# Kernel optimization log

Hardware: AMD Instinct MI355X
Metric: run time of the kernel (lower is better)

## Reference

```python
import jax, jax.numpy as jnp
import numpy as np

N_HEADS = 4

def setup_inputs() -> dict:
    key = jax.random.key(0)
    ks = jax.random.split(key, 9)
    B, C, H, W = 4, 256, 64, 64
    nh, hs = N_HEADS, C // N_HEADS
    s = 0.02
    return {
        "x": jax.random.normal(ks[0], (B, C, H, W), jnp.float32),
        "wq": jax.random.normal(ks[1], (C, C), jnp.float32) * s,
        "bq": jax.random.normal(ks[2], (C,), jnp.float32) * s,
        "wk": jax.random.normal(ks[3], (C, C), jnp.float32) * s,
        "bk": jax.random.normal(ks[4], (C,), jnp.float32) * s,
        "wv": jax.random.normal(ks[5], (C, C), jnp.float32) * s,
        "bv": jax.random.normal(ks[6], (C,), jnp.float32) * s,
        "rel_h": jax.random.normal(ks[7], (1, nh, hs, 1, H), jnp.float32),
        "rel_w": jax.random.normal(ks[8], (1, nh, hs, W, 1), jnp.float32),
    }

def reference(x, wq, bq, wk, bk, wv, bv, rel_h, rel_w):
    B, C, H, W = x.shape
    nh = N_HEADS
    hs = C // nh
    S = H * W

    def proj(w, b):
        # 1x1 conv == per-pixel linear over channels -> [B, C, H, W]
        y = jnp.einsum('oc,bchw->bohw', w, x) + b[None, :, None, None]
        # faithful to torch .view: flatten [C,H,W] row-major into [S, nh, hs]
        y = y.reshape(B, S, nh, hs)
        return y.transpose(0, 2, 1, 3)  # [B, nh, S, hs]

    q = proj(wq, bq)
    k = proj(wk, bk)
    v = proj(wv, bv)

    # content scores (NOTE: no 1/sqrt(d) scaling in BoT override)
    attn_content = jnp.einsum('bnqd,bnkd->bnqk', q, k)  # [B, nh, S, S]
    # learned relative position term: broadcast-add then flatten (w,h) order
    pos = (rel_h + rel_w).reshape(1, nh, hs, S)  # [1, nh, hs, S]
    attn_position = jnp.einsum('bnqd,ands->bnqs', q, pos)  # [B, nh, S, S]

    probs = jax.nn.softmax(attn_content + attn_position, axis=-1)
    ctx = jnp.einsum('bnqk,bnkd->bnqd', probs, v)  # [B, nh, S, hs]
    # faithful to torch: transpose(1,2) then view(B, C, width, height)
    out = ctx.transpose(0, 2, 1, 3).reshape(B, C, W, H)
    return out
```

## Files before the change

### kernel.cpp

```cpp
#include <hip/hip_runtime.h>
#include <hip/hip_bf16.h>
#include <stdint.h>
#include <math.h>

typedef __bf16 bf16_t;
typedef __bf16 bf16x8 __attribute__((ext_vector_type(8)));
typedef float  f32x4  __attribute__((ext_vector_type(4)));
typedef float  f32x16 __attribute__((ext_vector_type(16)));
typedef unsigned int u32;

#define S_SZ 4096
#define HS   64
#define OUT_B_STRIDE (256 * 64 * 64)
#define LOG2E 1.4426950408889634f

#define GLOAD_LDS(gsrc, ldst)                                                              \
    __builtin_amdgcn_global_load_lds((__attribute__((address_space(1))) void*)(void*)(gsrc), \
                                     (__attribute__((address_space(3))) void*)(void*)(ldst),  \
                                     16, 0, 0)

static __device__ __forceinline__ u32 pack2(__bf16 a, __bf16 b) {
    return (u32)__builtin_bit_cast(uint16_t, a) | ((u32)__builtin_bit_cast(uint16_t, b) << 16);
}

__global__ __launch_bounds__(256)
void prep_kernel(const float* __restrict__ wq, const float* __restrict__ wk,
                 const float* __restrict__ wv, const float* __restrict__ rel_h,
                 const float* __restrict__ rel_w,
                 bf16_t* __restrict__ Wh, bf16_t* __restrict__ Wl,
                 bf16_t* __restrict__ Rt)
{
    const int blk = blockIdx.x;
    if (blk < 768) {
        const int o = blk;
        const int c = threadIdx.x;
        const float* src = o < 256 ? wq : (o < 512 ? wk : wv);
        float v = src[(size_t)(o & 255) * 256 + c];
        if (o < 256) v *= LOG2E;
        __bf16 h = (__bf16)v;
        Wh[(size_t)o * 256 + c] = h;
        Wl[(size_t)o * 256 + c] = (__bf16)(v - (float)h);
    } else {
        const int e = (blk - 768) * 256 + threadIdx.x;
        const int n  = e >> 18;
        const int rr = e & 262143;
        const int t  = rr >> 6;
        const int d  = rr & 63;
        const int h2 = t >> 8, o = t & 255;
        float v = rel_h[(n * 64 + d) * 64 + (o & 3) * 16 + h2]
                + rel_w[(n * 64 + d) * 64 + (o >> 2)];
        Rt[e] = (bf16_t)v;
    }
}

__global__ __launch_bounds__(512, 2)
void proj_kernel(const float* __restrict__ x,
                 const bf16_t* __restrict__ Wh, const bf16_t* __restrict__ Wl,
                 const float* __restrict__ bq, const float* __restrict__ bk,
                 const float* __restrict__ bv, const bf16_t* __restrict__ Rt,
                 bf16_t* __restrict__ q_ws, bf16_t* __restrict__ k2_ws,
                 bf16_t* __restrict__ vt2_ws)
{
    const int bx = blockIdx.x;
    const int b  = bx >> 6;
    const int h  = bx & 63;
    const int p0 = h * 64;
    const int n  = h & 3;
    const int h2 = h >> 2;
    const int bn = b * 4 + n;
    const int tid = threadIdx.x;

    __shared__ __align__(16) char SM[65536];

    {
        const int cpair = tid & 127, pg = tid >> 7;
        const int c0 = cpair * 2;
        const float* x0 = x + ((size_t)b * 256 + c0) * 4096 + p0 + pg * 16;
        const int sub = (c0 >> 6) * 128;
        const int u   = (c0 >> 3) & 7;
        const int e2  = (c0 & 7) * 2;
        #pragma unroll
        for (int i4 = 0; i4 < 4; ++i4) {
            f32x4 ra = *(const f32x4*)(x0 + i4 * 4);
            f32x4 rb = *(const f32x4*)(x0 + 4096 + i4 * 4);
            #pragma unroll
            for (int i = 0; i < 4; ++i) {
                const int p = pg * 16 + i4 * 4 + i;
                __bf16 ha = (__bf16)ra[i], hb = (__bf16)rb[i];
                float  la = ra[i] - (float)ha, lb = rb[i] - (float)hb;
                const int off = p * 512 + sub + ((u ^ (p & 7)) * 16) + e2;
                *(u32*)(SM + off)         = pack2(ha, hb);
                *(u32*)(SM + 32768 + off) = pack2((__bf16)la, (__bf16)lb);
            }
        }
    }
    __syncthreads();

    const int wid = tid >> 6, lane = tid & 63, l31 = lane & 31, hi = lane >> 5;

    int obs[3], pjs[3];
    const bf16_t* whp[3];
    const bf16_t* wlp[3];
    #pragma unroll
    for (int j = 0; j < 3; ++j) {
        const int of = (wid * 3 + j) * 32;
        pjs[j] = of >> 8;
        obs[j] = of & 255;
        whp[j] = Wh + (size_t)(of + l31) * 256 + hi * 8;
        wlp[j] = Wl + (size_t)(of + l31) * 256 + hi * 8;
    }

    const char* XHp = SM + l31 * 512;
    const char* XLp = SM + 32768 + l31 * 512;

    f32x16 acc[3][2] = {};

    #pragma unroll
    for (int ks = 0; ks < 16; ++ks) {
        bf16x8 wh[3], wl[3];
        #pragma unroll
        for (int j = 0; j < 3; ++j) {
            wh[j] = *(const bf16x8*)(whp[j] + ks * 16);
            wl[j] = *(const bf16x8*)(wlp[j] + ks * 16);
        }
        const int rb_ = (ks >> 2) * 128 + ((((ks * 2 + hi) & 7) ^ (l31 & 7)) * 16);
        bf16x8 xh[2], xl[2];
        #pragma unroll
        for (int pt = 0; pt < 2; ++pt) {
            xh[pt] = *(const bf16x8*)(XHp + pt * 16384 + rb_);
            xl[pt] = *(const bf16x8*)(XLp + pt * 16384 + rb_);
        }
        #pragma unroll
        for (int j = 0; j < 3; ++j)
            #pragma unroll
            for (int pt = 0; pt < 2; ++pt) {
                acc[j][pt] = __builtin_amdgcn_mfma_f32_32x32x16_bf16(wh[j], xh[pt], acc[j][pt], 0, 0, 0);
                acc[j][pt] = __builtin_amdgcn_mfma_f32_32x32x16_bf16(wh[j], xl[pt], acc[j][pt], 0, 0, 0);
                acc[j][pt] = __builtin_amdgcn_mfma_f32_32x32x16_bf16(wl[j], xh[pt], acc[j][pt], 0, 0, 0);
            }
    }
    __syncthreads();

    f32x4 bias[3][2][4];
    #pragma unroll
    for (int j = 0; j < 3; ++j) {
        const float* bp = pjs[j] == 0 ? bq : (pjs[j] == 1 ? bk : bv);
        #pragma unroll
        for (int g2 = 0; g2 < 4; ++g2) {
            f32x4 v = *(const f32x4*)(bp + obs[j] + hi * 4 + g2 * 8);
            if (pjs[j] == 0) {
                #pragma unroll
                for (int i = 0; i < 4; ++i) v[i] *= LOG2E;
            }
            bias[j][0][g2] = v;  bias[j][1][g2] = v;
        }
    }

    #pragma unroll
    for (int j = 0; j < 3; ++j) {
        if (pjs[j] == 1) continue;
        #pragma unroll
        for (int pt = 0; pt < 2; ++pt) {
            const int d = pt * 32 + l31;
            #pragma unroll
            for (int g2 = 0; g2 < 4; ++g2)
                #pragma unroll
                for (int rr = 0; rr < 4; ++rr) {
                    const int o = obs[j] + rr + 4 * hi + 8 * g2;
                    const float v = acc[j][pt][g2 * 4 + rr] + bias[j][pt][g2][rr];
                    if (pjs[j] == 0) {
                        *(bf16_t*)(SM + o * 128 + d * 2) = (bf16_t)v;
                    } else {
                        *(bf16_t*)(SM + 32768 + d * 512 + ((o * 2) ^ ((d & 7) << 4))) = (bf16_t)v;
                    }
                }
        }
    }
    __syncthreads();
    {
        bf16_t* qp = q_ws + (size_t)bn * 4096 * 64;
        #pragma unroll
        for (int i = 0; i < 4; ++i) {
            const int c = i * 512 + tid;
            const int o = c >> 3, d8 = c & 7;
            uint4 v = *(const uint4*)(SM + c * 16);
            *(uint4*)(qp + (size_t)(o * 16 + h2) * 64 + d8 * 8) = v;
        }
        bf16_t* vp = vt2_ws + (size_t)bn * 64 * 4096 + h2 * 256;
        #pragma unroll
        for (int i = 0; i < 4; ++i) {
            const int c = i * 512 + tid;
            const int d = c >> 5, k = c & 31;
            uint4 v = *(const uint4*)(SM + 32768 + d * 512 + ((k * 16) ^ ((d & 7) << 4)));
            *(uint4*)(vp + (size_t)d * 4096 + k * 8) = v;
        }
    }
    __syncthreads();

    #pragma unroll
    for (int j = 0; j < 3; ++j) {
        if (pjs[j] != 1) continue;
        #pragma unroll
        for (int pt = 0; pt < 2; ++pt) {
            const int d = pt * 32 + l31;
            #pragma unroll
            for (int g2 = 0; g2 < 4; ++g2)
                #pragma unroll
                for (int rr = 0; rr < 4; ++rr) {
                    const int o = obs[j] + rr + 4 * hi + 8 * g2;
                    *(bf16_t*)(SM + o * 128 + d * 2) =
                        (bf16_t)(acc[j][pt][g2 * 4 + rr] + bias[j][pt][g2][rr]);
                }
        }
    }
    __syncthreads();
    {
        const bf16_t* Rp = Rt + ((size_t)n * 4096 + h2 * 256) * 64;
        bf16_t* kp = k2_ws + ((size_t)bn * 4096 + h2 * 256) * 64;
        #pragma unroll
        for (int i = 0; i < 4; ++i) {
            const int c = i * 512 + tid;
            bf16x8 kv = *(const bf16x8*)(SM + c * 16);
            bf16x8 rv = *(const bf16x8*)(Rp + c * 8);
            bf16x8 res;
            #pragma unroll
            for (int ii = 0; ii < 8; ++ii)
                res[ii] = (__bf16)((float)kv[ii] + (float)rv[ii]);
            *(bf16x8*)(kp + c * 8) = res;
        }
    }
}

__global__ __launch_bounds__(256, 2)
void attn_kernel(const bf16_t* __restrict__ q_ws, const bf16_t* __restrict__ k_ws,
                 const bf16_t* __restrict__ vt_ws, float* __restrict__ out)
{
    const int tid  = threadIdx.x;
    const int wid  = tid >> 6;
    const int lane = tid & 63;
    const int l31  = lane & 31;
    const int hi   = lane >> 5;

    const int wg  = blockIdx.x;
    const int swz = (wg & 7) * 64 + (wg >> 3);
    const int bn  = swz >> 5;
    const int qb  = swz & 31;
    const int b   = bn >> 2, n = bn & 3;

    __shared__ __align__(16) bf16_t Kt[4][64 * 64];
    __shared__ __align__(16) bf16_t Vt[4][64 * 64];

    const bf16_t* Qb = q_ws  + (size_t)bn * S_SZ * HS;
    const bf16_t* Kb = k_ws  + (size_t)bn * S_SZ * HS;
    const bf16_t* Vb = vt_ws + (size_t)bn * HS * S_SZ;

    const int c0 = wid * 64 + lane;
    const int ra = c0 >> 3, ga = (c0 & 7) ^ (ra & 7);
    const bf16_t* ksrcA = Kb + ra * HS + ga * 8;
    const bf16_t* ksrcB = ksrcA + 32 * HS;
    const bf16_t* vsrcA = Vb + (size_t)ra * S_SZ + ga * 8;
    const bf16_t* vsrcB = vsrcA + (size_t)32 * S_SZ;

#define STAGE(buf, ts)                                                        \
    GLOAD_LDS(ksrcA + (size_t)(ts) * 64 * HS, &Kt[buf][wid * 512]);           \
    GLOAD_LDS(ksrcB + (size_t)(ts) * 64 * HS, &Kt[buf][2048 + wid * 512]);    \
    GLOAD_LDS(vsrcA + (ts) * 64,              &Vt[buf][wid * 512]);           \
    GLOAD_LDS(vsrcB + (ts) * 64,              &Vt[buf][2048 + wid * 512]);

    const int q = qb * 128 + wid * 32 + l31;
    bf16x8 qf[4];
    #pragma unroll
    for (int dk = 0; dk < 4; ++dk)
        qf[dk] = *(const bf16x8*)(Qb + (size_t)q * HS + dk * 16 + hi * 8);

    f32x16 oacc[2];
    f32x16 Z16;
    #pragma unroll
    for (int i = 0; i < 16; ++i) { oacc[0][i] = 0.f; oacc[1][i] = 0.f; Z16[i] = 0.f; }
    float lsum = 0.f;

    const int swzme = (l31 & 7) << 4;

    STAGE(0, 0); STAGE(1, 1); STAGE(2, 2);
    asm volatile("s_waitcnt vmcnt(8)" ::: "memory");
    __builtin_amdgcn_s_barrier();
    asm volatile("" ::: "memory");

    for (int tb = 0; tb < 64; tb += 4) {
        #pragma unroll
        for (int u = 0; u < 4; ++u) {
            const int t = tb + u;
            {
                const int ts = (t + 3 > 63) ? 63 : t + 3;
                STAGE((u + 3) & 3, ts);
            }

            const char* Kbase = (const char*)&Kt[u][0] + l31 * 128;
            const char* Vbase = (const char*)&Vt[u][0] + l31 * 128;

            f32x16 sacc[2];
            __builtin_amdgcn_s_setprio(1);
            #pragma unroll
            for (int hh = 0; hh < 2; ++hh) {
                bf16x8 kf[4];
                #pragma unroll
                for (int dk = 0; dk < 4; ++dk)
                    kf[dk] = *(const bf16x8*)(Kbase + hh * 4096 + (((2 * dk + hi) * 16) ^ swzme));
                sacc[hh] = __builtin_amdgcn_mfma_f32_32x32x16_bf16(kf[0], qf[0], Z16, 0, 0, 0);
                #pragma unroll
                for (int dk = 1; dk < 4; ++dk)
                    sacc[hh] = __builtin_amdgcn_mfma_f32_32x32x16_bf16(kf[dk], qf[dk], sacc[hh], 0, 0, 0);
            }
            __builtin_amdgcn_s_setprio(0);

            u32 Wd[2][4][2];
            float ps[4] = {0.f, 0.f, 0.f, 0.f};
            #pragma unroll
            for (int hh = 0; hh < 2; ++hh)
                #pragma unroll
                for (int c = 0; c < 4; ++c)
                    #pragma unroll
                    for (int tt = 0; tt < 2; ++tt) {
                        float pa = __builtin_amdgcn_exp2f(sacc[hh][c * 4 + tt * 2]);
                        float pb = __builtin_amdgcn_exp2f(sacc[hh][c * 4 + tt * 2 + 1]);
                        ps[c] += pa + pb;
                        u32 w;
                        asm("v_cvt_pk_bf16_f32 %0, %1, %2" : "=v"(w) : "v"(pa), "v"(pb));
                        Wd[hh][c][tt] = w;
                    }
            lsum += (ps[0] + ps[1]) + (ps[2] + ps[3]);

            u32 F[4][4];
            #pragma unroll
            for (int hh = 0; hh < 2; ++hh)
                #pragma unroll
                for (int pr = 0; pr < 2; ++pr)
                    #pragma unroll
                    for (int tt = 0; tt < 2; ++tt) {
                        u32 a = Wd[hh][2 * pr][tt], bb = Wd[hh][2 * pr + 1][tt];
                        asm("v_permlane32_swap_b32 %0, %1" : "+v"(a), "+v"(bb));
                        F[2 * hh + pr][tt]     = a;
                        F[2 * hh + pr][2 + tt] = bb;
                    }

            __builtin_amdgcn_s_setprio(1);
            #pragma unroll
            for (int dh = 0; dh < 2; ++dh) {
                #pragma unroll
                for (int kk = 0; kk < 4; ++kk) {
                    bf16x8 vf = *(const bf16x8*)(Vbase + dh * 4096 + (((2 * kk + hi) * 16) ^ swzme));
                    union { u32 u[4]; bf16x8 v; } pf;
                    pf.u[0] = F[kk][0]; pf.u[1] = F[kk][1];
                    pf.u[2] = F[kk][2]; pf.u[3] = F[kk][3];
                    oacc[dh] = __builtin_amdgcn_mfma_f32_32x32x16_bf16(vf, pf.v, oacc[dh], 0, 0, 0);
                }
            }
            __builtin_amdgcn_s_setprio(0);

            asm volatile("s_waitcnt vmcnt(8)" ::: "memory");
            __builtin_amdgcn_s_barrier();
            asm volatile("" ::: "memory");
        }
    }
#undef STAGE

    float lt  = lsum + __shfl_xor(lsum, 32);
    float inv = 1.0f / lt;
    float* outp = out + (size_t)b * OUT_B_STRIDE + (size_t)q * 256 + n * 64;
    #pragma unroll
    for (int dh = 0; dh < 2; ++dh)
        #pragma unroll
        for (int g2 = 0; g2 < 4; ++g2) {
            f32x4 v4;
            #pragma unroll
            for (int r = 0; r < 4; ++r) v4[r] = oacc[dh][g2 * 4 + r] * inv;
            *(f32x4*)(outp + dh * 32 + g2 * 8 + hi * 4) = v4;
        }
}

extern "C" void kernel_launch(void* const* d_in, const int* in_sizes, int n_in,
                              void* d_out, int out_size, void* d_ws, size_t ws_size,
                              hipStream_t stream)
{
    const float* x     = (const float*)d_in[0];
    const float* wq    = (const float*)d_in[1];
    const float* bq    = (const float*)d_in[2];
    const float* wk    = (const float*)d_in[3];
    const float* bk    = (const float*)d_in[4];
    const float* wv    = (const float*)d_in[5];
    const float* bv    = (const float*)d_in[6];
    const float* rel_h = (const float*)d_in[7];
    const float* rel_w = (const float*)d_in[8];
    float* out = (float*)d_out;

    bf16_t* q_ws   = (bf16_t*)d_ws;
    bf16_t* k2_ws  = q_ws  + (size_t)16 * S_SZ * HS;
    bf16_t* vt2_ws = k2_ws + (size_t)16 * S_SZ * HS;

    bf16_t* end = (bf16_t*)d_out + (size_t)out_size * 2;
    bf16_t* Wl  = end - 196608;
    bf16_t* Wh  = Wl - 196608;
    bf16_t* Rt  = Wh - 1048576;

    prep_kernel<<<4864, 256, 0, stream>>>(wq, wk, wv, rel_h, rel_w, Wh, Wl, Rt);
    proj_kernel<<<256, 512, 0, stream>>>(x, Wh, Wl, bq, bk, bv, Rt,
                                         q_ws, k2_ws, vt2_ws);
    attn_kernel<<<512, 256, 0, stream>>>(q_ws, k2_ws, vt2_ws, out);
}
```

Baseline: 129.0 us.

## Software-pipeline QK with softmax-PV, merge proj epilogue stages, shrink prep grid

```diff
diff --git a/kernel.cpp b/kernel.cpp
--- a/kernel.cpp
+++ b/kernel.cpp
@@ -31,25 +31,42 @@
                  bf16_t* __restrict__ Rt)
 {
     const int blk = blockIdx.x;
-    if (blk < 768) {
-        const int o = blk;
-        const int c = threadIdx.x;
-        const float* src = o < 256 ? wq : (o < 512 ? wk : wv);
-        float v = src[(size_t)(o & 255) * 256 + c];
-        if (o < 256) v *= LOG2E;
-        __bf16 h = (__bf16)v;
-        Wh[(size_t)o * 256 + c] = h;
-        Wl[(size_t)o * 256 + c] = (__bf16)(v - (float)h);
+    if (blk < 48) {
+        const int base = blk * 4096;
+        #pragma unroll
+        for (int i = 0; i < 16; ++i) {
+            const int e = base + i * 256 + threadIdx.x;
+            const int o = e >> 8, c = e & 255;
+            const float* src = o < 256 ? wq : (o < 512 ? wk : wv);
+            float v = src[(size_t)(o & 255) * 256 + c];
+            if (o < 256) v *= LOG2E;
+            __bf16 h = (__bf16)v;
+            Wh[e] = h;
+            Wl[e] = (__bf16)(v - (float)h);
+        }
     } else {
-        const int e = (blk - 768) * 256 + threadIdx.x;
-        const int n  = e >> 18;
-        const int rr = e & 262143;
-        const int t  = rr >> 6;
-        const int d  = rr & 63;
-        const int h2 = t >> 8, o = t & 255;
-        float v = rel_h[(n * 64 + d) * 64 + (o & 3) * 16 + h2]
-                + rel_w[(n * 64 + d) * 64 + (o >> 2)];
-        Rt[e] = (bf16_t)v;
+        const int rb = blk - 48;
+        const int n = rb >> 4, h2 = rb & 15;
+        __shared__ float rh[4096], rw[4096];
+        for (int i = threadIdx.x; i < 4096; i += 256) {
+            rh[i] = rel_h[n * 4096 + i];
+            rw[i] = rel_w[n * 4096 + i];
+        }
+        __syncthreads();
+        bf16_t* Rp = Rt + ((size_t)n * 4096 + h2 * 256) * 64;
+        const int d0 = (threadIdx.x & 7) * 8;
+        const int ob = threadIdx.x >> 3;
+        #pragma unroll
+        for (int i = 0; i < 8; ++i) {
+            const int o  = i * 32 + ob;
+            const int ih = (o & 3) * 16 + h2;
+            const int iw = o >> 2;
+            bf16x8 rv;
+            #pragma unroll
+            for (int dd = 0; dd < 8; ++dd)
+                rv[dd] = (bf16_t)(rh[(d0 + dd) * 64 + ih] + rw[(d0 + dd) * 64 + iw]);
+            *(bf16x8*)(Rp + (size_t)o * 64 + d0) = rv;
+        }
     }
 }
 
@@ -70,7 +87,7 @@
     const int bn = b * 4 + n;
     const int tid = threadIdx.x;
 
-    __shared__ __align__(16) char SM[65536];
+    __shared__ __align__(16) char SM[98304];
 
     {
         const int cpair = tid & 127, pg = tid >> 7;
@@ -141,24 +158,18 @@
     }
     __syncthreads();
 
-    f32x4 bias[3][2][4];
     #pragma unroll
     for (int j = 0; j < 3; ++j) {
         const float* bp = pjs[j] == 0 ? bq : (pjs[j] == 1 ? bk : bv);
+        f32x4 bv4[4];
         #pragma unroll
         for (int g2 = 0; g2 < 4; ++g2) {
-            f32x4 v = *(const f32x4*)(bp + obs[j] + hi * 4 + g2 * 8);
+            bv4[g2] = *(const f32x4*)(bp + obs[j] + hi * 4 + g2 * 8);
             if (pjs[j] == 0) {
                 #pragma unroll
-                for (int i = 0; i < 4; ++i) v[i] *= LOG2E;
+                for (int i = 0; i < 4; ++i) bv4[g2][i] *= LOG2E;
             }
-            bias[j][0][g2] = v;  bias[j][1][g2] = v;
-        }
-    }
-
-    #pragma unroll
-    for (int j = 0; j < 3; ++j) {
-        if (pjs[j] == 1) continue;
+        }
         #pragma unroll
         for (int pt = 0; pt < 2; ++pt) {
             const int d = pt * 32 + l31;
@@ -167,16 +178,19 @@
                 #pragma unroll
                 for (int rr = 0; rr < 4; ++rr) {
                     const int o = obs[j] + rr + 4 * hi + 8 * g2;
-                    const float v = acc[j][pt][g2 * 4 + rr] + bias[j][pt][g2][rr];
+                    const float v = acc[j][pt][g2 * 4 + rr] + bv4[g2][rr];
                     if (pjs[j] == 0) {
                         *(bf16_t*)(SM + o * 128 + d * 2) = (bf16_t)v;
+                    } else if (pjs[j] == 2) {
+                        *(bf16_t*)(SM + 32768 + d * 512 + ((o * 2) ^ ((d & 7) << 4))) = (bf16_t)v;
                     } else {
-                        *(bf16_t*)(SM + 32768 + d * 512 + ((o * 2) ^ ((d & 7) << 4))) = (bf16_t)v;
+                        *(bf16_t*)(SM + 65536 + o * 128 + d * 2) = (bf16_t)v;
                     }
                 }
         }
     }
     __syncthreads();
+
     {
         bf16_t* qp = q_ws + (size_t)bn * 4096 * 64;
         #pragma unroll
@@ -194,33 +208,12 @@
             uint4 v = *(const uint4*)(SM + 32768 + d * 512 + ((k * 16) ^ ((d & 7) << 4)));
             *(uint4*)(vp + (size_t)d * 4096 + k * 8) = v;
         }
-    }
-    __syncthreads();
-
-    #pragma unroll
-    for (int j = 0; j < 3; ++j) {
-        if (pjs[j] != 1) continue;
-        #pragma unroll
-        for (int pt = 0; pt < 2; ++pt) {
-            const int d = pt * 32 + l31;
-            #pragma unroll
-            for (int g2 = 0; g2 < 4; ++g2)
-                #pragma unroll
-                for (int rr = 0; rr < 4; ++rr) {
-                    const int o = obs[j] + rr + 4 * hi + 8 * g2;
-                    *(bf16_t*)(SM + o * 128 + d * 2) =
-                        (bf16_t)(acc[j][pt][g2 * 4 + rr] + bias[j][pt][g2][rr]);
-                }
-        }
-    }
-    __syncthreads();
-    {
         const bf16_t* Rp = Rt + ((size_t)n * 4096 + h2 * 256) * 64;
         bf16_t* kp = k2_ws + ((size_t)bn * 4096 + h2 * 256) * 64;
         #pragma unroll
         for (int i = 0; i < 4; ++i) {
             const int c = i * 512 + tid;
-            bf16x8 kv = *(const bf16x8*)(SM + c * 16);
+            bf16x8 kv = *(const bf16x8*)(SM + 65536 + c * 16);
             bf16x8 rv = *(const bf16x8*)(Rp + c * 8);
             bf16x8 res;
             #pragma unroll
@@ -281,87 +274,88 @@
 
     const int swzme = (l31 & 7) << 4;
 
+#define QKPAIR(DST, BUF)                                                               \
+    { const char* Kb_ = (const char*)&Kt[BUF][0] + l31 * 128;                          \
+      __builtin_amdgcn_s_setprio(1);                                                   \
+      _Pragma("unroll")                                                                \
+      for (int hh = 0; hh < 2; ++hh) {                                                 \
+          bf16x8 kf[4];                                                                \
+          _Pragma("unroll")                                                            \
+          for (int dk = 0; dk < 4; ++dk)                                               \
+              kf[dk] = *(const bf16x8*)(Kb_ + hh * 4096 + (((2 * dk + hi) * 16) ^ swzme)); \
+          DST[hh] = __builtin_amdgcn_mfma_f32_32x32x16_bf16(kf[0], qf[0], Z16, 0, 0, 0);   \
+          _Pragma("unroll")                                                            \
+          for (int dk = 1; dk < 4; ++dk)                                               \
+              DST[hh] = __builtin_amdgcn_mfma_f32_32x32x16_bf16(kf[dk], qf[dk], DST[hh], 0, 0, 0); \
+      }                                                                                \
+      __builtin_amdgcn_s_setprio(0); }
+
+#define EXPPV(SRC, VBUF)                                                               \
+    { u32 Wd[2][4][2];                                                                 \
+      float ps[4] = {0.f, 0.f, 0.f, 0.f};                                              \
+      _Pragma("unroll")                                                                \
+      for (int hh = 0; hh < 2; ++hh)                                                   \
+      _Pragma("unroll")                                                                \
+      for (int c = 0; c < 4; ++c)                                                      \
+      _Pragma("unroll")                                                                \
+      for (int tt = 0; tt < 2; ++tt) {                                                 \
+          float pa = __builtin_amdgcn_exp2f(SRC[hh][c * 4 + tt * 2]);                  \
+          float pb = __builtin_amdgcn_exp2f(SRC[hh][c * 4 + tt * 2 + 1]);              \
+          ps[c] += pa + pb;                                                            \
+          u32 w_;                                                                      \
+          asm("v_cvt_pk_bf16_f32 %0, %1, %2" : "=v"(w_) : "v"(pa), "v"(pb));           \
+          Wd[hh][c][tt] = w_; }                                                        \
+      lsum += (ps[0] + ps[1]) + (ps[2] + ps[3]);                                       \
+      u32 F[4][4];                                                                     \
+      _Pragma("unroll")                                                                \
+      for (int hh = 0; hh < 2; ++hh)                                                   \
+      _Pragma("unroll")                                                                \
+      for (int pr = 0; pr < 2; ++pr)                                                   \
+      _Pragma("unroll")                                                                \
+      for (int tt = 0; tt < 2; ++tt) {                                                 \
+          u32 a_ = Wd[hh][2 * pr][tt], b_ = Wd[hh][2 * pr + 1][tt];                    \
+          asm("v_permlane32_swap_b32 %0, %1" : "+v"(a_), "+v"(b_));                    \
+          F[2 * hh + pr][tt]     = a_;                                                 \
+          F[2 * hh + pr][2 + tt] = b_; }                                               \
+      const char* Vb_ = (const char*)&Vt[VBUF][0] + l31 * 128;                         \
+      __builtin_amdgcn_s_setprio(1);                                                   \
+      _Pragma("unroll")                                                                \
+      for (int dh = 0; dh < 2; ++dh)                                                   \
+      _Pragma("unroll")                                                                \
+      for (int kk = 0; kk < 4; ++kk) {                                                 \
+          bf16x8 vf = *(const bf16x8*)(Vb_ + dh * 4096 + (((2 * kk + hi) * 16) ^ swzme)); \
+          union { u32 u[4]; bf16x8 v; } pf;                                            \
+          pf.u[0] = F[kk][0]; pf.u[1] = F[kk][1]; pf.u[2] = F[kk][2]; pf.u[3] = F[kk][3]; \
+          oacc[dh] = __builtin_amdgcn_mfma_f32_32x32x16_bf16(vf, pf.v, oacc[dh], 0, 0, 0); } \
+      __builtin_amdgcn_s_setprio(0); }
+
+#define ITER(U, SC, SN)                                                                \
+    { asm volatile("s_waitcnt vmcnt(4)" ::: "memory");                                 \
+      __builtin_amdgcn_s_barrier();                                                    \
+      asm volatile("" ::: "memory");                                                   \
+      { const int t_ = tb + (U);                                                       \
+        const int ts_ = (t_ + 3 > 63) ? 63 : t_ + 3;                                   \
+        STAGE(((U) + 3) & 3, ts_); }                                                   \
+      QKPAIR(SN, ((U) + 1) & 3);                                                       \
+      EXPPV(SC, (U) & 3); }
+
     STAGE(0, 0); STAGE(1, 1); STAGE(2, 2);
     asm volatile("s_waitcnt vmcnt(8)" ::: "memory");
     __builtin_amdgcn_s_barrier();
     asm volatile("" ::: "memory");
 
+    f32x16 S0[2], S1[2];
+    QKPAIR(S0, 0);
+
     for (int tb = 0; tb < 64; tb += 4) {
-        #pragma unroll
-        for (int u = 0; u < 4; ++u) {
-            const int t = tb + u;
-            {
-                const int ts = (t + 3 > 63) ? 63 : t + 3;
-                STAGE((u + 3) & 3, ts);
-            }
-
-            const char* Kbase = (const char*)&Kt[u][0] + l31 * 128;
-            const char* Vbase = (const char*)&Vt[u][0] + l31 * 128;
-
-            f32x16 sacc[2];
-            __builtin_amdgcn_s_setprio(1);
-            #pragma unroll
-            for (int hh = 0; hh < 2; ++hh) {
-                bf16x8 kf[4];
-                #pragma unroll
-                for (int dk = 0; dk < 4; ++dk)
-                    kf[dk] = *(const bf16x8*)(Kbase + hh * 4096 + (((2 * dk + hi) * 16) ^ swzme));
-                sacc[hh] = __builtin_amdgcn_mfma_f32_32x32x16_bf16(kf[0], qf[0], Z16, 0, 0, 0);
-                #pragma unroll
-                for (int dk = 1; dk < 4; ++dk)
-                    sacc[hh] = __builtin_amdgcn_mfma_f32_32x32x16_bf16(kf[dk], qf[dk], sacc[hh], 0, 0, 0);
-            }
-            __builtin_amdgcn_s_setprio(0);
-
-            u32 Wd[2][4][2];
-            float ps[4] = {0.f, 0.f, 0.f, 0.f};
-            #pragma unroll
-            for (int hh = 0; hh < 2; ++hh)
-                #pragma unroll
-                for (int c = 0; c < 4; ++c)
-                    #pragma unroll
-                    for (int tt = 0; tt < 2; ++tt) {
-                        float pa = __builtin_amdgcn_exp2f(sacc[hh][c * 4 + tt * 2]);
-                        float pb = __builtin_amdgcn_exp2f(sacc[hh][c * 4 + tt * 2 + 1]);
-                        ps[c] += pa + pb;
-                        u32 w;
-                        asm("v_cvt_pk_bf16_f32 %0, %1, %2" : "=v"(w) : "v"(pa), "v"(pb));
-                        Wd[hh][c][tt] = w;
-                    }
-            lsum += (ps[0] + ps[1]) + (ps[2] + ps[3]);
-
-            u32 F[4][4];
-            #pragma unroll
-            for (int hh = 0; hh < 2; ++hh)
-                #pragma unroll
-                for (int pr = 0; pr < 2; ++pr)
-                    #pragma unroll
-                    for (int tt = 0; tt < 2; ++tt) {
-                        u32 a = Wd[hh][2 * pr][tt], bb = Wd[hh][2 * pr + 1][tt];
-                        asm("v_permlane32_swap_b32 %0, %1" : "+v"(a), "+v"(bb));
-                        F[2 * hh + pr][tt]     = a;
-                        F[2 * hh + pr][2 + tt] = bb;
-                    }
-
-            __builtin_amdgcn_s_setprio(1);
-            #pragma unroll
-            for (int dh = 0; dh < 2; ++dh) {
-                #pragma unroll
-                for (int kk = 0; kk < 4; ++kk) {
-                    bf16x8 vf = *(const bf16x8*)(Vbase + dh * 4096 + (((2 * kk + hi) * 16) ^ swzme));
-                    union { u32 u[4]; bf16x8 v; } pf;
-                    pf.u[0] = F[kk][0]; pf.u[1] = F[kk][1];
-                    pf.u[2] = F[kk][2]; pf.u[3] = F[kk][3];
-                    oacc[dh] = __builtin_amdgcn_mfma_f32_32x32x16_bf16(vf, pf.v, oacc[dh], 0, 0, 0);
-                }
-            }
-            __builtin_amdgcn_s_setprio(0);
-
-            asm volatile("s_waitcnt vmcnt(8)" ::: "memory");
-            __builtin_amdgcn_s_barrier();
-            asm volatile("" ::: "memory");
-        }
-    }
+        ITER(0, S0, S1);
+        ITER(1, S1, S0);
+        ITER(2, S0, S1);
+        ITER(3, S1, S0);
+    }
+#undef ITER
+#undef EXPPV
+#undef QKPAIR
 #undef STAGE
 
     float lt  = lsum + __shfl_xor(lsum, 32);
@@ -402,7 +396,7 @@
     bf16_t* Wh  = Wl - 196608;
     bf16_t* Rt  = Wh - 1048576;
 
-    prep_kernel<<<4864, 256, 0, stream>>>(wq, wk, wv, rel_h, rel_w, Wh, Wl, Rt);
+    prep_kernel<<<112, 256, 0, stream>>>(wq, wk, wv, rel_h, rel_w, Wh, Wl, Rt);
     proj_kernel<<<256, 512, 0, stream>>>(x, Wh, Wl, bq, bk, bv, Rt,
                                          q_ws, k2_ws, vt2_ws);
     attn_kernel<<<512, 256, 0, stream>>>(q_ws, k2_ws, vt2_ws, out);
```

After: 134.5 us. +4.3%, slower.
